# Kernel tuning notes

Hardware: AMD Instinct MI355X
Metric: run time of the kernel (lower is better)

Reference implementation:

```python
import jax, jax.numpy as jnp
import numpy as np

E = 524288
IN = 256
OUT = 256
T = 16


def setup_inputs() -> dict:
    key = jax.random.key(0)
    k1, k2, k3 = jax.random.split(key, 3)
    x_j = jax.random.normal(k1, (E, IN), dtype=jnp.float32)
    # kaiming-uniform-ish init for the per-type weights
    bound = 1.0 / np.sqrt(IN)
    rel_weights = jax.random.uniform(k2, (T, IN, OUT), dtype=jnp.float32,
                                     minval=-bound, maxval=bound)
    edge_types = jax.random.randint(k3, (E,), 0, T, dtype=jnp.int64)
    return {"x_j": x_j, "rel_weights": rel_weights, "edge_types": edge_types}


def reference(x_j, rel_weights, edge_types):
    # Faithful to the torch semantics:
    #   out[i] = x_j[edge_types[i]] @ rel_weights[edge_types[i]]
    # (the torch code's broadcasted matmul + [i, edge_types[i]] gather reduces
    #  to a per-type matvec followed by an index gather).
    num_types = rel_weights.shape[0]
    # y[t] = x_j[t] @ W[t], shape [T, OUT] -- tiny compute
    y = jnp.einsum('ti,tio->to', x_j[:num_types], rel_weights)
    # memory-bound gather to [E, OUT]
    return y[edge_types]
```

## Files before the change

### kernel.cpp

```cpp
#include <hip/hip_runtime.h>


#define RL_IN  256
#define RL_OUT 256
#define RL_T   16

typedef float f32x4 __attribute__((ext_vector_type(4)));

__global__ __launch_bounds__(1024)
void rl_compute_y(const float* __restrict__ x,
                  const float* __restrict__ W,
                  float* __restrict__ y) {
    const int t = blockIdx.x;
    const int c = threadIdx.x >> 8;
    const int o = threadIdx.x & 255;
    const int i0 = c * 64;

    __shared__ float xs[RL_IN];
    if (threadIdx.x < RL_IN) xs[threadIdx.x] = x[t * RL_IN + threadIdx.x];
    __syncthreads();

    const float* Wt = W + (size_t)t * RL_IN * RL_OUT + (size_t)i0 * RL_OUT;
    float acc = 0.0f;
#pragma unroll 8
    for (int i = 0; i < 64; ++i) {
        acc += xs[i0 + i] * Wt[i * RL_OUT + o];
    }

    __shared__ float part[4][RL_OUT];
    part[c][o] = acc;
    __syncthreads();
    if (c == 0) {
        y[t * RL_OUT + o] = part[0][o] + part[1][o] + part[2][o] + part[3][o];
    }
}

__global__ __launch_bounds__(256)
void rl_gather(const int* __restrict__ et,
               const f32x4* __restrict__ y4,
               f32x4* __restrict__ out4,
               int E) {
    __shared__ f32x4 ys[RL_T * (RL_OUT / 4)];
    __shared__ int tys[256];

    for (int i = threadIdx.x; i < RL_T * (RL_OUT / 4); i += blockDim.x)
        ys[i] = y4[i];
    __syncthreads();

    const int lane       = threadIdx.x & 63;
    const int waveBase   = threadIdx.x & ~63;
    const int wave       = blockIdx.x * (blockDim.x >> 6) + (threadIdx.x >> 6);
    const int totalWaves = gridDim.x * (blockDim.x >> 6);

    for (int base = wave * 64; base < E; base += totalWaves * 64) {
        tys[waveBase + lane] = et[base + lane];

        if (base + 64 <= E) {
#pragma unroll 8
            for (int r = 0; r < 64; ++r) {
                const int t = tys[waveBase + r];
                out4[(size_t)(base + r) * 64 + lane] = ys[t * 64 + lane];
            }
        } else {
            for (int r = 0; base + r < E; ++r) {
                const int t = tys[waveBase + r];
                out4[(size_t)(base + r) * 64 + lane] = ys[t * 64 + lane];
            }
        }
    }
}

extern "C" void kernel_launch(void* const* d_in, const int* in_sizes, int n_in,
                              void* d_out, int out_size, void* d_ws, size_t ws_size,
                              hipStream_t stream) {
    const float* x_j  = (const float*)d_in[0];
    const float* W    = (const float*)d_in[1];
    const int*   et   = (const int*)d_in[2];
    float*       out  = (float*)d_out;

    const int E = in_sizes[2];

    float* y = (float*)d_ws;

    rl_compute_y<<<RL_T, 1024, 0, stream>>>(x_j, W, y);

    rl_gather<<<2048, 256, 0, stream>>>(et, (const f32x4*)y,
                                        (f32x4*)out, E);
}
```

Measured before the change: 108.3 us.

## Hold type table in registers, group rows by ballot, use nontemporal stores

The gather kernel now keeps each lane's slice of the 16-row result table in registers instead of shared memory, so there is no LDS staging and no block barrier. For each 64-edge chunk it runs a ballot per type and writes every matching row from the register copy, which removes the per-row shared-memory index and value reads. Output stores become nontemporal to avoid polluting caches with the 512 MB write stream. The cost is 64 extra vector registers per thread, a 16-iteration ballot loop with data-dependent inner loops, and a separate path for the ragged tail.

```diff
diff --git a/kernel.cpp b/kernel.cpp
--- a/kernel.cpp
+++ b/kernel.cpp
@@ -40,33 +40,39 @@
                const f32x4* __restrict__ y4,
                f32x4* __restrict__ out4,
                int E) {
-    __shared__ f32x4 ys[RL_T * (RL_OUT / 4)];
-    __shared__ int tys[256];
-
-    for (int i = threadIdx.x; i < RL_T * (RL_OUT / 4); i += blockDim.x)
-        ys[i] = y4[i];
-    __syncthreads();
-
     const int lane       = threadIdx.x & 63;
-    const int waveBase   = threadIdx.x & ~63;
     const int wave       = blockIdx.x * (blockDim.x >> 6) + (threadIdx.x >> 6);
     const int totalWaves = gridDim.x * (blockDim.x >> 6);
 
-    for (int base = wave * 64; base < E; base += totalWaves * 64) {
-        tys[waveBase + lane] = et[base + lane];
+    f32x4 y16[RL_T];
+#pragma unroll
+    for (int t = 0; t < RL_T; ++t)
+        y16[t] = y4[t * 64 + lane];
 
-        if (base + 64 <= E) {
-#pragma unroll 8
-            for (int r = 0; r < 64; ++r) {
-                const int t = tys[waveBase + r];
-                out4[(size_t)(base + r) * 64 + lane] = ys[t * 64 + lane];
-            }
-        } else {
-            for (int r = 0; base + r < E; ++r) {
-                const int t = tys[waveBase + r];
-                out4[(size_t)(base + r) * 64 + lane] = ys[t * 64 + lane];
+    for (long base = (long)wave * 64; base + 64 <= E; base += (long)totalWaves * 64) {
+        const int tv = et[base + lane];
+        f32x4* __restrict__ dst = out4 + (size_t)base * 64;
+
+#pragma unroll
+        for (int t = 0; t < RL_T; ++t) {
+            unsigned long long m = __ballot(tv == t);
+            const f32x4 v = y16[t];
+            while (m) {
+                const int r = __builtin_ctzll(m);
+                m &= m - 1;
+                __builtin_nontemporal_store(v, &dst[r * 64 + lane]);
             }
         }
+    }
+
+    const long tail = (long)(E & ~63LL);
+    for (long row = tail + wave; row < E; row += totalWaves) {
+        const int t = et[row];
+        f32x4 v;
+#pragma unroll
+        for (int tt = 0; tt < RL_T; ++tt)
+            if (tt == t) v = y16[tt];
+        __builtin_nontemporal_store(v, &out4[(size_t)row * 64 + lane]);
     }
 }
 
```

Result: no change. 107.7 us (-0.5%).
